# Performance work log

Hardware: AMD Instinct MI355X
Metric: run time of the kernel (lower is better)

The kernel has to match this reference:

```python
import jax, jax.numpy as jnp
import numpy as np

N_HEADS = 16


def setup_inputs() -> dict:
    key = jax.random.key(0)
    ks = jax.random.split(key, 8)
    ts, td, b, hc = 64, 4096, 8, 1024
    scale = 1.0 / np.sqrt(hc)
    return {
        "s": jax.random.normal(ks[0], (ts, b, hc), dtype=jnp.float32),
        "d": jax.random.normal(ks[1], (td, b, hc), dtype=jnp.float32),
        "Wq": jax.random.normal(ks[2], (hc, hc), dtype=jnp.float32) * scale,
        "bq": jax.random.normal(ks[3], (hc,), dtype=jnp.float32) * 0.01,
        "Wk": jax.random.normal(ks[4], (hc, hc), dtype=jnp.float32) * scale,
        "bk": jax.random.normal(ks[5], (hc,), dtype=jnp.float32) * 0.01,
        "Wv": jax.random.normal(ks[6], (hc, hc), dtype=jnp.float32) * scale,
        "bv": jax.random.normal(ks[7], (hc,), dtype=jnp.float32) * 0.01,
    }


def reference(s, d, Wq, bq, Wk, bk, Wv, bv):
    ts, b, hc = s.shape
    td = d.shape[0]
    h = N_HEADS
    c = hc // h
    # linear projections (torch Linear: x @ W.T + b)
    q = (s @ Wq.T + bq).reshape(ts, b, h, c)
    k = (d @ Wk.T + bk).reshape(td, b, h, c)
    v = (d @ Wv.T + bv).reshape(td, b, h, c)
    # scores over (slot, token) pairs, scaled
    a = jnp.einsum('sbhc,dbhc->sdbh', q, k) / jnp.sqrt(jnp.asarray(c, s.dtype))
    # competitive softmax across the SLOT axis (dim 0), not the key axis
    a = jax.nn.softmax(a, axis=0)          # (ts, td, b, h)
    n = jnp.sum(a, axis=1) + 0.001         # (ts, b, h)
    num = jnp.einsum('sdbh,dbhc->sbhc', a, v)
    out = num / n[..., None]               # normalized weighted average
    return out.reshape(ts, b, hc)
```

## Files before the change

### kernel.cpp

```cpp
#include <hip/hip_runtime.h>


#define TS 64
#define TD 4096
#define BATCH 8
#define HC 1024
#define NHEAD 16
#define MD (TD*BATCH)
#define MS (TS*BATCH)
#define NCHUNK 8
#define CHTOK (TD/NCHUNK)

#define KTILES 32

typedef __attribute__((ext_vector_type(8))) __bf16 bf16x8;
typedef __attribute__((ext_vector_type(4))) float f32x4;
typedef __attribute__((ext_vector_type(4))) unsigned short u16x4;
typedef __attribute__((ext_vector_type(8))) unsigned short u16x8;

__device__ __forceinline__ unsigned short f2bf(float x){
  union { float f; unsigned u; } v; v.f = x;
  unsigned r = v.u + 0x7FFFu + ((v.u >> 16) & 1u);
  return (unsigned short)(r >> 16);
}

__device__ __forceinline__ void gll16(const void* g, void* l){
  __builtin_amdgcn_global_load_lds((__attribute__((address_space(1))) void*)g,
                                   (__attribute__((address_space(3))) void*)l, 16, 0, 0);
}

__global__ void cvt_bf16(const float* __restrict__ in, unsigned short* __restrict__ out, int n4){
  int i = blockIdx.x * blockDim.x + threadIdx.x;
  if (i >= n4) return;
  f32x4 f = ((const f32x4*)in)[i];
  u16x4 o;
  o[0] = f2bf(f[0]); o[1] = f2bf(f[1]); o[2] = f2bf(f[2]); o[3] = f2bf(f[3]);
  ((u16x4*)out)[i] = o;
}

__global__ __launch_bounds__(512, 2) void gemm_kv(
    const unsigned short* __restrict__ A,
    const unsigned short* __restrict__ W,
    const float* __restrict__ bk,
    const float* __restrict__ bv,
    unsigned short* __restrict__ Kout,
    unsigned short* __restrict__ Vout)
{
  __shared__ unsigned short As[4][256*32];
  __shared__ unsigned short Bs[4][256*32];

  const int nwg = gridDim.x;
  const int cpx = nwg >> 3;
  const int orig = blockIdx.x;
  const int wg = (orig & 7) * cpx + (orig >> 3);
  const int mt = wg >> 3, nt = wg & 7;
  const int tid = threadIdx.x;
  const int lane = tid & 63, w = tid >> 6;
  const int l15 = lane & 15, lg = lane >> 4;
  const int wm = w >> 2, wn = w & 3;

  const int lr = lane >> 2;
  const int schunk = (((lane & 3) ^ ((lane >> 3) & 3)) << 4);
  const char* pa[2]; const char* pb[2]; unsigned ldso[2];
  #pragma unroll
  for (int j = 0; j < 2; ++j){
    int grow = j*128 + w*16 + lr;
    pa[j] = (const char*)A + (size_t)(mt*256 + grow)*2048 + schunk;
    pb[j] = (const char*)W + (size_t)(nt*256 + grow)*2048 + schunk;
    ldso[j] = (unsigned)(j*8192 + w*1024);
  }

  #define STAGE_A(t) { char* dst = (char*)&As[(t)&3][0]; \
    gll16(pa[0] + (size_t)(t)*64, dst + ldso[0]); \
    gll16(pa[1] + (size_t)(t)*64, dst + ldso[1]); }
  #define STAGE_B(t) { char* dst = (char*)&Bs[(t)&3][0]; \
    gll16(pb[0] + (size_t)(t)*64, dst + ldso[0]); \
    gll16(pb[1] + (size_t)(t)*64, dst + ldso[1]); }

  const unsigned cswz = ((unsigned)(lg ^ ((l15 >> 1) & 3))) << 4;
  const unsigned aoff = (unsigned)(wm*128 + l15)*64 + cswz;
  const unsigned boff = (unsigned)(wn*64  + l15)*64 + cswz;

  const f32x4 fz = {0.f, 0.f, 0.f, 0.f};
  f32x4 acc[8][4];
  #pragma unroll
  for (int m = 0; m < 8; ++m)
    #pragma unroll
    for (int n = 0; n < 4; ++n) acc[m][n] = fz;

  STAGE_A(0) STAGE_B(0) STAGE_A(1) STAGE_B(1) STAGE_A(2) STAGE_B(2)
  asm volatile("s_waitcnt vmcnt(8)" ::: "memory");
  __builtin_amdgcn_s_barrier();
  __builtin_amdgcn_sched_barrier(0);

  for (int t = 0; t < KTILES; ++t){
    const char* as = (const char*)&As[t & 3][0];
    const char* bs = (const char*)&Bs[t & 3][0];

    bf16x8 af0[4], bfr[4];
    #pragma unroll
    for (int mf = 0; mf < 4; ++mf) af0[mf] = *(const bf16x8*)(as + aoff + mf*1024u);
    #pragma unroll
    for (int nf = 0; nf < 4; ++nf) bfr[nf] = *(const bf16x8*)(bs + boff + nf*1024u);
    if (t + 3 < KTILES) STAGE_A(t + 3)
    __builtin_amdgcn_s_setprio(1);
    #pragma unroll
    for (int mf = 0; mf < 4; ++mf)
      #pragma unroll
      for (int nf = 0; nf < 4; ++nf)
        acc[mf][nf] = __builtin_amdgcn_mfma_f32_16x16x32_bf16(af0[mf], bfr[nf], acc[mf][nf], 0, 0, 0);
    __builtin_amdgcn_s_setprio(0);

    bf16x8 af1[4];
    #pragma unroll
    for (int mf = 0; mf < 4; ++mf) af1[mf] = *(const bf16x8*)(as + aoff + (4 + mf)*1024u);
    if (t + 3 < KTILES) STAGE_B(t + 3)
    __builtin_amdgcn_s_setprio(1);
    #pragma unroll
    for (int mf = 0; mf < 4; ++mf)
      #pragma unroll
      for (int nf = 0; nf < 4; ++nf)
        acc[4 + mf][nf] = __builtin_amdgcn_mfma_f32_16x16x32_bf16(af1[mf], bfr[nf], acc[4 + mf][nf], 0, 0, 0);
    __builtin_amdgcn_s_setprio(0);

    __builtin_amdgcn_sched_barrier(0);
    if (t < KTILES - 3)       { asm volatile("s_waitcnt vmcnt(8)" ::: "memory"); }
    else if (t == KTILES - 3) { asm volatile("s_waitcnt vmcnt(4)" ::: "memory"); }
    else if (t == KTILES - 2) { asm volatile("s_waitcnt vmcnt(0)" ::: "memory"); }
    __builtin_amdgcn_s_barrier();
    __builtin_amdgcn_sched_barrier(0);
  }

  const int ccol = (nt & 3)*256 + wn*64;
  unsigned short* Cb = (nt < 4) ? Kout : Vout;
  const float* bias = (nt < 4) ? bk : bv;
  float bvv[4];
  #pragma unroll
  for (int nf = 0; nf < 4; ++nf) bvv[nf] = bias[ccol + nf*16 + l15];
  #pragma unroll
  for (int mf = 0; mf < 8; ++mf){
    #pragma unroll
    for (int r = 0; r < 4; ++r){
      size_t row = (size_t)(mt*256 + wm*128 + mf*16 + lg*4 + r);
      unsigned short* cp = Cb + row*1024 + ccol;
      #pragma unroll
      for (int nf = 0; nf < 4; ++nf)
        cp[nf*16 + l15] = f2bf(acc[mf][nf][r] + bvv[nf]);
    }
  }
  #undef STAGE_A
  #undef STAGE_B
}

__global__ __launch_bounds__(256) void gemm128(
    const unsigned short* __restrict__ A,
    const unsigned short* __restrict__ W,
    const float* __restrict__ bias,
    unsigned short* __restrict__ C)
{
  __shared__ unsigned short As[128*64];
  __shared__ unsigned short Bs[128*64];
  const int nwg = gridDim.x;
  const int cpx = nwg >> 3;
  const int orig = blockIdx.x;
  const int wg = (orig & 7) * cpx + (orig >> 3);
  const int mt = wg >> 3, nt = wg & 7;
  const int tid = threadIdx.x;
  const int lane = tid & 63, w = tid >> 6;
  const int l15 = lane & 15, lg = lane >> 4;
  const int wr = w >> 1, wc = w & 1;

  const int lrow = lane >> 3;
  const int lch  = (lane & 7) << 4;
  const char* pA[4]; const char* pB[4]; unsigned ldsoff[4];
  #pragma unroll
  for (int j = 0; j < 4; ++j){
    int row = w*32 + j*8 + lrow;
    int sw  = lch ^ ((row & 7) << 4);
    pA[j] = (const char*)A + (size_t)(mt*128 + row) * 2048 + sw;
    pB[j] = (const char*)W + (size_t)(nt*128 + row) * 2048 + sw;
    ldsoff[j] = (unsigned)(w*32 + j*8) * 128;
  }

  const f32x4 fz = {0.f, 0.f, 0.f, 0.f};
  f32x4 acc[4][4];
  #pragma unroll
  for (int m = 0; m < 4; ++m)
    #pragma unroll
    for (int n = 0; n < 4; ++n) acc[m][n] = fz;

  for (int kt = 0; kt < 16; ++kt){
    __syncthreads();
    #pragma unroll
    for (int j = 0; j < 4; ++j){
      gll16(pA[j] + (size_t)kt*128, (char*)As + ldsoff[j]);
      gll16(pB[j] + (size_t)kt*128, (char*)Bs + ldsoff[j]);
    }
    __syncthreads();
    #pragma unroll
    for (int kk = 0; kk < 2; ++kk){
      bf16x8 af[4], bfr[4];
      #pragma unroll
      for (int m = 0; m < 4; ++m){
        int row = wr*64 + m*16 + l15;
        af[m] = *(const bf16x8*)((const char*)As + row*128 + ((lg*16 + kk*64) ^ ((row & 7) << 4)));
      }
      #pragma unroll
      for (int n = 0; n < 4; ++n){
        int row = wc*64 + n*16 + l15;
        bfr[n] = *(const bf16x8*)((const char*)Bs + row*128 + ((lg*16 + kk*64) ^ ((row & 7) << 4)));
      }
      #pragma unroll
      for (int m = 0; m < 4; ++m)
        #pragma unroll
        for (int n = 0; n < 4; ++n)
          acc[m][n] = __builtin_amdgcn_mfma_f32_16x16x32_bf16(af[m], bfr[n], acc[m][n], 0, 0, 0);
    }
  }

  const int ccol0 = nt*128 + wc*64;
  float bv[4];
  #pragma unroll
  for (int n = 0; n < 4; ++n) bv[n] = bias[ccol0 + n*16 + l15];
  #pragma unroll
  for (int m = 0; m < 4; ++m){
    #pragma unroll
    for (int r = 0; r < 4; ++r){
      size_t row = (size_t)(mt*128 + wr*64 + m*16 + lg*4 + r);
      unsigned short* cp = C + row*1024 + ccol0;
      #pragma unroll
      for (int n = 0; n < 4; ++n)
        cp[n*16 + l15] = f2bf(acc[m][n][r] + bv[n]);
    }
  }
}

__global__ __launch_bounds__(256) void attn_kernel(
    const unsigned short* __restrict__ Q,
    const unsigned short* __restrict__ K,
    const unsigned short* __restrict__ V,
    float* __restrict__ P)
{
  __shared__ unsigned short Qs[64*64];
  __shared__ unsigned short Ks[64*64];
  __shared__ unsigned short Vt[80*64];
  __shared__ unsigned short Al[64*64];
  __shared__ float red[256];

  const int bh = blockIdx.x;
  const int chunk = blockIdx.y;
  const int bb = bh >> 4, h = bh & 15;
  const int tid = threadIdx.x;
  const int lane = tid & 63, w = tid >> 6;
  const int l15 = lane & 15, lg = lane >> 4;
  const int lrow = lane >> 3, lch = (lane & 7) << 4;

  for (int i = tid; i < 16*64; i += 256){
    int r = i >> 6;
    Vt[(64 + r)*64 + (i & 63)] = (r == 0) ? (unsigned short)0x3F80 : (unsigned short)0;
  }

  #pragma unroll
  for (int j = 0; j < 2; ++j){
    int row = w*16 + j*8 + lrow;
    int sw = lch ^ ((row & 7) << 4);
    const char* g = (const char*)Q + (size_t)(row*BATCH + bb)*2048 + h*128 + sw;
    gll16(g, (char*)Qs + (w*16 + j*8)*128);
  }

  const f32x4 fz = {0.f, 0.f, 0.f, 0.f};
  f32x4 acc[5];
  #pragma unroll
  for (int nb = 0; nb < 5; ++nb) acc[nb] = fz;

  const int vtok = tid >> 2;
  const int vcg  = tid & 3;
  const int t0 = chunk * CHTOK;

  for (int tt = 0; tt < CHTOK/64; ++tt){
    const int tb = t0 + tt*64;
    #pragma unroll
    for (int j = 0; j < 2; ++j){
      int row = w*16 + j*8 + lrow;
      int sw = lch ^ ((row & 7) << 4);
      const char* g = (const char*)K + (size_t)((size_t)(tb + row)*BATCH + bb)*2048 + h*128 + sw;
      gll16(g, (char*)Ks + (w*16 + j*8)*128);
    }
    const char* vg = (const char*)V + (size_t)((size_t)(tb + vtok)*BATCH + bb)*2048 + h*128 + vcg*32;
    u16x8 v0 = *(const u16x8*)vg;
    u16x8 v1 = *(const u16x8*)(vg + 16);
    __syncthreads();

    bf16x8 qa[2];
    #pragma unroll
    for (int kk = 0; kk < 2; ++kk){
      int row = w*16 + l15;
      qa[kk] = *(const bf16x8*)((const char*)Qs + row*128 + ((lg*16 + kk*64) ^ ((row & 7) << 4)));
    }
    float e[4][4];
    #pragma unroll
    for (int nb = 0; nb < 4; ++nb){
      f32x4 s = fz;
      #pragma unroll
      for (int kk = 0; kk < 2; ++kk){
        int row = nb*16 + l15;
        bf16x8 kb = *(const bf16x8*)((const char*)Ks + row*128 + ((lg*16 + kk*64) ^ ((row & 7) << 4)));
        s = __builtin_amdgcn_mfma_f32_16x16x32_bf16(qa[kk], kb, s, 0, 0, 0);
      }
      #pragma unroll
      for (int r = 0; r < 4; ++r) e[nb][r] = __expf(s[r] * 0.125f);
    }
    #pragma unroll
    for (int nb = 0; nb < 4; ++nb){
      float cp = e[nb][0] + e[nb][1] + e[nb][2] + e[nb][3];
      cp += __shfl_xor(cp, 16);
      cp += __shfl_xor(cp, 32);
      if (lg == 0) red[w*64 + nb*16 + l15] = cp;
    }
    __syncthreads();

    #pragma unroll
    for (int nb = 0; nb < 4; ++nb){
      int col = nb*16 + l15;
      float dn = red[col] + red[64 + col] + red[128 + col] + red[192 + col];
      float inv = 1.0f / dn;
      #pragma unroll
      for (int r = 0; r < 4; ++r){
        int row = w*16 + lg*4 + r;
        Al[row*64 + ((((2*col)) ^ ((row & 7) << 4)) >> 1)] = f2bf(e[nb][r] * inv);
      }
    }
    #pragma unroll
    for (int ee = 0; ee < 8; ++ee){
      int c0 = vcg*16 + ee;
      int sw0 = (((c0 & 7) ^ (c0 >> 3)) & 7) << 4;
      Vt[c0*64 + (((2*vtok) ^ sw0) >> 1)] = v0[ee];
    }
    #pragma unroll
    for (int ee = 0; ee < 8; ++ee){
      int c1 = vcg*16 + 8 + ee;
      int sw1 = (((c1 & 7) ^ (c1 >> 3)) & 7) << 4;
      Vt[c1*64 + (((2*vtok) ^ sw1) >> 1)] = v1[ee];
    }
    __syncthreads();

    bf16x8 aa[2];
    #pragma unroll
    for (int kk = 0; kk < 2; ++kk){
      int row = w*16 + l15;
      aa[kk] = *(const bf16x8*)((const char*)Al + row*128 + ((lg*16 + kk*64) ^ ((row & 7) << 4)));
    }
    #pragma unroll
    for (int nb = 0; nb < 5; ++nb){
      #pragma unroll
      for (int kk = 0; kk < 2; ++kk){
        int row = nb*16 + l15;
        int sw = (((row & 7) ^ (row >> 3)) & 7) << 4;
        bf16x8 vb = *(const bf16x8*)((const char*)Vt + row*128 + ((lg*16 + kk*64) ^ sw));
        acc[nb] = __builtin_amdgcn_mfma_f32_16x16x32_bf16(aa[kk], vb, acc[nb], 0, 0, 0);
      }
    }
  }

  float* Pb = P + (size_t)(bh*NCHUNK + chunk) * 64 * 80;
  #pragma unroll
  for (int nb = 0; nb < 5; ++nb){
    #pragma unroll
    for (int r = 0; r < 4; ++r){
      int s = w*16 + lg*4 + r;
      Pb[(size_t)s*80 + nb*16 + l15] = acc[nb][r];
    }
  }
}

__global__ void reduce_out(const float* __restrict__ P, float* __restrict__ out){
  int flat = blockIdx.x * 256 + threadIdx.x;
  int c = flat & 63, s = (flat >> 6) & 63, bh = flat >> 12;
  int bb = bh >> 4, h = bh & 15;
  float sc = 0.f, sn = 0.f;
  #pragma unroll
  for (int ch = 0; ch < NCHUNK; ++ch){
    const float* base = P + ((size_t)(bh*NCHUNK + ch)*64 + s)*80;
    sc += base[c];
    sn += base[64];
  }
  out[((size_t)s*BATCH + bb)*1024 + h*64 + c] = sc / (sn + 0.001f);
}

extern "C" void kernel_launch(void* const* d_in, const int* in_sizes, int n_in,
                              void* d_out, int out_size, void* d_ws, size_t ws_size,
                              hipStream_t stream)
{
  const float* s  = (const float*)d_in[0];
  const float* d  = (const float*)d_in[1];
  const float* Wq = (const float*)d_in[2];
  const float* bq = (const float*)d_in[3];
  const float* Wk = (const float*)d_in[4];
  const float* bk = (const float*)d_in[5];
  const float* Wv = (const float*)d_in[6];
  const float* bv = (const float*)d_in[7];
  float* out = (float*)d_out;

  char* ws = (char*)d_ws;
  unsigned short* dbf = (unsigned short*)(ws);
  unsigned short* sbf = (unsigned short*)(ws + 67108864);
  unsigned short* wqb = (unsigned short*)(ws + 68157440);
  unsigned short* wkb = (unsigned short*)(ws + 70254592);
  unsigned short* wvb = (unsigned short*)(ws + 72351744);
  unsigned short* Qw  = (unsigned short*)(ws + 74448896);
  unsigned short* Kw  = (unsigned short*)(ws + 75497472);
  unsigned short* Vw  = (unsigned short*)(ws + 142606336);
  float*          Pw  = (float*)(ws + 209715200);

  (void)in_sizes; (void)n_in; (void)out_size; (void)ws_size;

  cvt_bf16<<<(MD*HC/4 + 255)/256, 256, 0, stream>>>(d,  dbf, MD*HC/4);
  cvt_bf16<<<(MS*HC/4 + 255)/256, 256, 0, stream>>>(s,  sbf, MS*HC/4);
  cvt_bf16<<<(HC*HC/4 + 255)/256, 256, 0, stream>>>(Wq, wqb, HC*HC/4);
  cvt_bf16<<<(HC*HC/4 + 255)/256, 256, 0, stream>>>(Wk, wkb, HC*HC/4);
  cvt_bf16<<<(HC*HC/4 + 255)/256, 256, 0, stream>>>(Wv, wvb, HC*HC/4);

  gemm128<<<(MS/128)*8, 256, 0, stream>>>(sbf, wqb, bq, Qw);
  gemm_kv<<<(MD/256)*8, 512, 0, stream>>>(dbf, wkb, bk, bv, Kw, Vw);

  attn_kernel<<<dim3(128, NCHUNK), 256, 0, stream>>>(Qw, Kw, Vw, Pw);

  reduce_out<<<(TS*BATCH*HC)/256, 256, 0, stream>>>(Pw, out);
}
```

Measured before the change: 254.0 us.

## Double-buffer LDS fragments in registers across K tiles of projection GEMM

Restructures the K/V projection GEMM main loop into a two-tile ping-pong. The next tile's A/B fragments are read from shared memory into a second register set while MFMAs run on the current set. A and B global-to-LDS stages are merged into one issue per tile, and the vmcnt waits are adjusted to match. The aim is to hide LDS read latency behind the MFMAs, at the cost of many more live fragment registers, which could reduce occupancy or cause spills.

```diff
diff --git a/kernel.cpp b/kernel.cpp
--- a/kernel.cpp
+++ b/kernel.cpp
@@ -70,17 +70,45 @@
     ldso[j] = (unsigned)(j*8192 + w*1024);
   }
 
-  #define STAGE_A(t) { char* dst = (char*)&As[(t)&3][0]; \
-    gll16(pa[0] + (size_t)(t)*64, dst + ldso[0]); \
-    gll16(pa[1] + (size_t)(t)*64, dst + ldso[1]); }
-  #define STAGE_B(t) { char* dst = (char*)&Bs[(t)&3][0]; \
-    gll16(pb[0] + (size_t)(t)*64, dst + ldso[0]); \
-    gll16(pb[1] + (size_t)(t)*64, dst + ldso[1]); }
+  #define STAGE_AB(t) { \
+    char* da = (char*)&As[(t)&3][0]; \
+    char* db = (char*)&Bs[(t)&3][0]; \
+    gll16(pa[0] + (size_t)(t)*64, da + ldso[0]); \
+    gll16(pa[1] + (size_t)(t)*64, da + ldso[1]); \
+    gll16(pb[0] + (size_t)(t)*64, db + ldso[0]); \
+    gll16(pb[1] + (size_t)(t)*64, db + ldso[1]); }
 
   const unsigned cswz = ((unsigned)(lg ^ ((l15 >> 1) & 3))) << 4;
   const unsigned aoff = (unsigned)(wm*128 + l15)*64 + cswz;
   const unsigned boff = (unsigned)(wn*64  + l15)*64 + cswz;
 
+  struct FragSet { bf16x8 a[8]; bf16x8 b[4]; };
+  FragSet FA, FB;
+
+  #define READ_FRAGS(F, slot) { \
+    const char* as_ = (const char*)&As[(slot)][0]; \
+    const char* bs_ = (const char*)&Bs[(slot)][0]; \
+    _Pragma("unroll") \
+    for (int mf = 0; mf < 8; ++mf) F.a[mf] = *(const bf16x8*)(as_ + aoff + mf*1024u); \
+    _Pragma("unroll") \
+    for (int nf = 0; nf < 4; ++nf) F.b[nf] = *(const bf16x8*)(bs_ + boff + nf*1024u); }
+
+  #define DO_MFMA(F) { \
+    __builtin_amdgcn_s_setprio(1); \
+    _Pragma("unroll") \
+    for (int mf = 0; mf < 8; ++mf) \
+      _Pragma("unroll") \
+      for (int nf = 0; nf < 4; ++nf) \
+        acc[mf][nf] = __builtin_amdgcn_mfma_f32_16x16x32_bf16(F.a[mf], F.b[nf], acc[mf][nf], 0, 0, 0); \
+    __builtin_amdgcn_s_setprio(0); }
+
+  #define BOUNDARY(t) { \
+    __builtin_amdgcn_sched_barrier(0); \
+    if ((t) < KTILES - 3)       { asm volatile("s_waitcnt vmcnt(4)" ::: "memory"); } \
+    else if ((t) == KTILES - 3) { asm volatile("s_waitcnt vmcnt(0)" ::: "memory"); } \
+    __builtin_amdgcn_s_barrier(); \
+    __builtin_amdgcn_sched_barrier(0); }
+
   const f32x4 fz = {0.f, 0.f, 0.f, 0.f};
   f32x4 acc[8][4];
   #pragma unroll
@@ -88,47 +116,23 @@
     #pragma unroll
     for (int n = 0; n < 4; ++n) acc[m][n] = fz;
 
-  STAGE_A(0) STAGE_B(0) STAGE_A(1) STAGE_B(1) STAGE_A(2) STAGE_B(2)
-  asm volatile("s_waitcnt vmcnt(8)" ::: "memory");
+  STAGE_AB(0) STAGE_AB(1) STAGE_AB(2)
+  asm volatile("s_waitcnt vmcnt(4)" ::: "memory");
   __builtin_amdgcn_s_barrier();
   __builtin_amdgcn_sched_barrier(0);
-
-  for (int t = 0; t < KTILES; ++t){
-    const char* as = (const char*)&As[t & 3][0];
-    const char* bs = (const char*)&Bs[t & 3][0];
-
-    bf16x8 af0[4], bfr[4];
-    #pragma unroll
-    for (int mf = 0; mf < 4; ++mf) af0[mf] = *(const bf16x8*)(as + aoff + mf*1024u);
-    #pragma unroll
-    for (int nf = 0; nf < 4; ++nf) bfr[nf] = *(const bf16x8*)(bs + boff + nf*1024u);
-    if (t + 3 < KTILES) STAGE_A(t + 3)
-    __builtin_amdgcn_s_setprio(1);
-    #pragma unroll
-    for (int mf = 0; mf < 4; ++mf)
-      #pragma unroll
-      for (int nf = 0; nf < 4; ++nf)
-        acc[mf][nf] = __builtin_amdgcn_mfma_f32_16x16x32_bf16(af0[mf], bfr[nf], acc[mf][nf], 0, 0, 0);
-    __builtin_amdgcn_s_setprio(0);
-
-    bf16x8 af1[4];
-    #pragma unroll
-    for (int mf = 0; mf < 4; ++mf) af1[mf] = *(const bf16x8*)(as + aoff + (4 + mf)*1024u);
-    if (t + 3 < KTILES) STAGE_B(t + 3)
-    __builtin_amdgcn_s_setprio(1);
-    #pragma unroll
-    for (int mf = 0; mf < 4; ++mf)
-      #pragma unroll
-      for (int nf = 0; nf < 4; ++nf)
-        acc[4 + mf][nf] = __builtin_amdgcn_mfma_f32_16x16x32_bf16(af1[mf], bfr[nf], acc[4 + mf][nf], 0, 0, 0);
-    __builtin_amdgcn_s_setprio(0);
-
-    __builtin_amdgcn_sched_barrier(0);
-    if (t < KTILES - 3)       { asm volatile("s_waitcnt vmcnt(8)" ::: "memory"); }
-    else if (t == KTILES - 3) { asm volatile("s_waitcnt vmcnt(4)" ::: "memory"); }
-    else if (t == KTILES - 2) { asm volatile("s_waitcnt vmcnt(0)" ::: "memory"); }
-    __builtin_amdgcn_s_barrier();
-    __builtin_amdgcn_sched_barrier(0);
+  READ_FRAGS(FA, 0)
+
+  #pragma unroll 1
+  for (int tp = 0; tp < KTILES/2; ++tp){
+    const int t = tp*2;
+    if (t + 3 < KTILES) STAGE_AB(t + 3)
+    READ_FRAGS(FB, (t+1) & 3)
+    DO_MFMA(FA)
+    BOUNDARY(t)
+    if (t + 4 < KTILES) STAGE_AB(t + 4)
+    if (t + 2 < KTILES) READ_FRAGS(FA, (t+2) & 3)
+    DO_MFMA(FB)
+    BOUNDARY(t + 1)
   }
 
   const int ccol = (nt & 3)*256 + wn*64;
@@ -148,8 +152,10 @@
         cp[nf*16 + l15] = f2bf(acc[mf][nf][r] + bvv[nf]);
     }
   }
-  #undef STAGE_A
-  #undef STAGE_B
+  #undef STAGE_AB
+  #undef READ_FRAGS
+  #undef DO_MFMA
+  #undef BOUNDARY
 }
 
 __global__ __launch_bounds__(256) void gemm128(
```

Result: slower. 274.5 us (+8.1%).
